# Performance work log

Hardware: AMD Instinct MI355X
Metric: run time of the kernel (lower is better)

Reference implementation:

```python
import jax, jax.numpy as jnp
import numpy as np

DN = ('NCHW', 'OIHW', 'NCHW')

def _conv(x, w, b=None):
    # x: [P, C, H, W], w: [1, C, k, k] -> [P, 1, H, W] with SAME padding
    y = jax.lax.conv_general_dilated(x, w, (1, 1), 'SAME', dimension_numbers=DN)
    if b is not None:
        y = y + b[None, :, None, None]
    return y

def setup_inputs() -> dict:
    key = jax.random.key(0)
    ks = jax.random.split(key, 6)
    T, P, H, W = 36, 64, 128, 256
    K = 5
    inputs = jax.random.normal(ks[0], (T, P, H, W), dtype=jnp.float32)
    w_reset = 0.1 * jax.random.normal(ks[1], (1, 2, K, K), dtype=jnp.float32)
    b_reset = jnp.zeros((1,), dtype=jnp.float32)
    w_update = 0.1 * jax.random.normal(ks[2], (1, 2, K, K), dtype=jnp.float32)
    b_update = jnp.zeros((1,), dtype=jnp.float32)
    w_out = 0.1 * jax.random.normal(ks[3], (1, 2, K, K), dtype=jnp.float32)
    gam = jnp.ones((P,), dtype=jnp.float32)
    add_weights = 0.02 * jax.random.normal(ks[4], (P, H, W), dtype=jnp.float32)
    bias = jnp.zeros((H, W), dtype=jnp.float32)
    return {"inputs": inputs, "w_reset": w_reset, "b_reset": b_reset,
            "w_update": w_update, "b_update": b_update, "w_out": w_out,
            "gam": gam, "add_weights": add_weights, "bias": bias}

def reference(inputs, w_reset, b_reset, w_update, b_update, w_out, gam, add_weights, bias):
    # inputs: [T, P, H, W]; renormalize by per-plant scale gam
    x = gam[None, :, None, None] * inputs
    x = x[:, :, None]  # [T, P, 1, H, W] (channel dim = 1)
    h0 = jnp.zeros_like(x[0])  # [P, 1, H, W]

    def step(h, xt):
        stacked = jnp.concatenate([xt, h], axis=1)  # [P, 2, H, W]
        u = jax.nn.sigmoid(_conv(stacked, w_update, b_update))  # update gate
        r = jax.nn.sigmoid(_conv(stacked, w_reset, b_reset))    # reset gate
        c = _conv(jnp.concatenate([xt, r * h], axis=1), w_out)  # candidate (no bias, no act)
        h_new = h * (1.0 - u) + c * u
        return h_new, h_new

    _, states = jax.lax.scan(step, h0, x)  # [T, P, 1, H, W]
    s = states[:, :, 0]  # [T, P, H, W]
    # final layer (additive=False, rnn_act=None): tanh then per-plant spatial weights
    xs = jnp.tanh(s) * add_weights[None]
    out_y = xs.sum(axis=1) + bias[None]  # [T, H, W]
    return out_y, xs
```

## Files before the change

### kernel.cpp

```cpp
#include <hip/hip_runtime.h>

constexpr int T = 36, P = 64, H = 128, W = 256;
constexpr int HW  = H * W;
constexpr int PHW = P * HW;

constexpr int TH   = 16;
constexpr int NB   = 8;
constexpr int NBLK = P * NB;
constexpr int SR = 25, SC = 268;
constexpr int RR = 20;

constexpr long long TMO_ARRIVE = 3000000;
constexpr long long TMO_STEP   = 1000000;

typedef float vfloat4 __attribute__((ext_vector_type(4)));

__device__ __forceinline__ float fast_sigmoid(float z) {
    float e = __expf(-z);
    return __builtin_amdgcn_rcpf(1.0f + e);
}
__device__ __forceinline__ float fast_tanh(float x) {
    float e = __expf(-2.0f * fabsf(x));
    float t = (1.0f - e) * __builtin_amdgcn_rcpf(1.0f + e);
    return copysignf(t, x);
}

__device__ __forceinline__ void lds_store4(float* d, float4 v) {
    *(float2*)d       = make_float2(v.x, v.y);
    *(float2*)(d + 2) = make_float2(v.z, v.w);
}

__global__ __launch_bounds__(512, 4) void gru_all(
    const float* __restrict__ inputs, const float* __restrict__ gam,
    const float* __restrict__ w_update, const float* __restrict__ b_update,
    const float* __restrict__ w_reset,  const float* __restrict__ b_reset,
    const float* __restrict__ w_out,    const float* __restrict__ add_w,
    float* __restrict__ xs, float* __restrict__ hhalo, int* __restrict__ flags)
{
    __shared__ __align__(16) float sx[SR][SC];
    __shared__ __align__(16) float sh[SR][SC];
    __shared__ __align__(16) float srh[RR][SC];
    __shared__ int s_nowait;

    const int tid  = threadIdx.x;
    const int bid  = blockIdx.x;
    const int p    = bid >> 3;
    const int band = bid & 7;
    const int y0   = band * TH;

    const float gamma = gam[p];
    const float bu = b_update[0];
    const float br = b_reset[0];

    const int cg = tid & 63, rbb = tid >> 6;
    const int ox = 4 * cg,   oy  = 2 * rbb;

    if (tid == 0) {
        s_nowait = 0;
        __hip_atomic_fetch_add(&flags[NBLK], 1, __ATOMIC_RELAXED, __HIP_MEMORY_SCOPE_AGENT);
        const long long t0 = (long long)__builtin_amdgcn_s_memrealtime();
        while (__hip_atomic_load(&flags[NBLK], __ATOMIC_RELAXED, __HIP_MEMORY_SCOPE_AGENT) < NBLK) {
            __builtin_amdgcn_s_sleep(16);
            if ((long long)__builtin_amdgcn_s_memrealtime() - t0 > TMO_ARRIVE) { s_nowait = 1; break; }
        }
    }

    float4 aw4[2];
    #pragma unroll
    for (int k = 0; k < 2; ++k)
        aw4[k] = *(const float4*)&add_w[(size_t)p * HW + (y0 + oy + k) * W + ox];

    for (int s = tid; s < SR * SC; s += 512) {
        (&sx[0][0])[s] = 0.f;
        (&sh[0][0])[s] = 0.f;
    }
    __syncthreads();
    {
        const float* xt = inputs + (size_t)p * HW;
        #pragma unroll
        for (int k = 0; k < 3; ++k) {
            const int s = tid + 512 * k;
            const int r = s >> 6, c4 = s & 63;
            const int gy = y0 + r - 4;
            if ((unsigned)gy < (unsigned)H) {
                float4 v = *(const float4*)&xt[gy * W + 4 * c4];
                v.x *= gamma; v.y *= gamma; v.z *= gamma; v.w *= gamma;
                lds_store4(&sx[r][6 + 4 * c4], v);
            }
        }
    }
    __syncthreads();

    #pragma unroll 1
    for (int t = 0; t < T; ++t) {
        float4 xp[3];
        {
            const int tc = (t + 1 < T) ? t + 1 : t;
            const float* xtn = inputs + (size_t)tc * PHW + (size_t)p * HW;
            #pragma unroll
            for (int k = 0; k < 3; ++k) {
                const int s = tid + 512 * k;
                const int r = s >> 6, c4 = s & 63;
                const int gy = y0 + r - 4;
                xp[k] = make_float4(0.f, 0.f, 0.f, 0.f);
                if ((unsigned)gy < (unsigned)H)
                    xp[k] = *(const float4*)&xtn[gy * W + 4 * c4];
            }
        }

        if (tid < 462) {
            const int b  = tid / 66;
            const int g  = tid - 66 * b;
            const int r0 = 3 * b;
            const int c0 = 4 * g;
            float racc[3][4], hold[3][4];
            #pragma unroll
            for (int k = 0; k < 3; ++k)
                #pragma unroll
                for (int c = 0; c < 4; ++c) racc[k][c] = br;
            #pragma unroll
            for (int ir = 0; ir < 7; ++ir) {
                const float4 xa = *(const float4*)&sx[r0 + ir][c0];
                const float4 xb = *(const float4*)&sx[r0 + ir][c0 + 4];
                const float4 ha = *(const float4*)&sh[r0 + ir][c0];
                const float4 hb = *(const float4*)&sh[r0 + ir][c0 + 4];
                const float vx[8] = {xa.x, xa.y, xa.z, xa.w, xb.x, xb.y, xb.z, xb.w};
                const float vh[8] = {ha.x, ha.y, ha.z, ha.w, hb.x, hb.y, hb.z, hb.w};
                if (ir >= 2 && ir <= 4) {
                    #pragma unroll
                    for (int c = 0; c < 4; ++c) hold[ir - 2][c] = vh[c + 2];
                }
                #pragma unroll
                for (int k = 0; k < 3; ++k) {
                    const int dy = ir - k;
                    if (dy >= 0 && dy <= 4) {
                        #pragma unroll
                        for (int dx = 0; dx < 5; ++dx) {
                            const float wx = w_reset[dy * 5 + dx];
                            const float wh = w_reset[25 + dy * 5 + dx];
                            #pragma unroll
                            for (int c = 0; c < 4; ++c) {
                                racc[k][c] = fmaf(vx[c + dx], wx, racc[k][c]);
                                racc[k][c] = fmaf(vh[c + dx], wh, racc[k][c]);
                            }
                        }
                    }
                }
            }
            #pragma unroll
            for (int k = 0; k < 3; ++k) {
                if (r0 + k < RR) {
                    float4 v;
                    v.x = fast_sigmoid(racc[k][0]) * hold[k][0];
                    v.y = fast_sigmoid(racc[k][1]) * hold[k][1];
                    v.z = fast_sigmoid(racc[k][2]) * hold[k][2];
                    v.w = fast_sigmoid(racc[k][3]) * hold[k][3];
                    lds_store4(&srh[r0 + k][c0 + 2], v);
                }
            }
        }
        __syncthreads();

        float4 hn4[2];
        {
            float uacc[2][4], cacc[2][4], hold[2][4];
            #pragma unroll
            for (int k = 0; k < 2; ++k)
                #pragma unroll
                for (int c = 0; c < 4; ++c) { uacc[k][c] = bu; cacc[k][c] = 0.f; }
            #pragma unroll
            for (int ir = 0; ir < 6; ++ir) {
                const int sr = oy + 2 + ir;
                const float4 xa = *(const float4*)&sx[sr][ox + 4];
                const float4 xb = *(const float4*)&sx[sr][ox + 8];
                const float4 ha = *(const float4*)&sh[sr][ox + 4];
                const float4 hb = *(const float4*)&sh[sr][ox + 8];
                const float4 ra = *(const float4*)&srh[oy + ir][ox + 4];
                const float4 rb = *(const float4*)&srh[oy + ir][ox + 8];
                const float vx[8] = {xa.x, xa.y, xa.z, xa.w, xb.x, xb.y, xb.z, xb.w};
                const float vh[8] = {ha.x, ha.y, ha.z, ha.w, hb.x, hb.y, hb.z, hb.w};
                const float vr[8] = {ra.x, ra.y, ra.z, ra.w, rb.x, rb.y, rb.z, rb.w};
                if (ir == 2) {
                    #pragma unroll
                    for (int c = 0; c < 4; ++c) hold[0][c] = vh[c + 2];
                }
                if (ir == 3) {
                    #pragma unroll
                    for (int c = 0; c < 4; ++c) hold[1][c] = vh[c + 2];
                }
                #pragma unroll
                for (int k = 0; k < 2; ++k) {
                    const int dy = ir - k;
                    if (dy >= 0 && dy <= 4) {
                        #pragma unroll
                        for (int dx = 0; dx < 5; ++dx) {
                            const float wux = w_update[dy * 5 + dx];
                            const float wuh = w_update[25 + dy * 5 + dx];
                            const float wox = w_out[dy * 5 + dx];
                            const float wor = w_out[25 + dy * 5 + dx];
                            #pragma unroll
                            for (int c = 0; c < 4; ++c) {
                                uacc[k][c] = fmaf(vx[c + dx], wux, uacc[k][c]);
                                uacc[k][c] = fmaf(vh[c + dx], wuh, uacc[k][c]);
                                cacc[k][c] = fmaf(vx[c + dx], wox, cacc[k][c]);
                                cacc[k][c] = fmaf(vr[c + dx], wor, cacc[k][c]);
                            }
                        }
                    }
                }
            }
            #pragma unroll
            for (int k = 0; k < 2; ++k) {
                float hn[4];
                #pragma unroll
                for (int c = 0; c < 4; ++c) {
                    const float u = fast_sigmoid(uacc[k][c]);
                    hn[c] = hold[k][c] + (cacc[k][c] - hold[k][c]) * u;
                }
                hn4[k] = make_float4(hn[0], hn[1], hn[2], hn[3]);
            }
        }
        __syncthreads();

        if (t + 1 < T && (rbb < 2 || rbb >= 6)) {
            float* hb = hhalo + (size_t)(t & 1) * (NBLK * 2048) + (size_t)bid * 2048;
            #pragma unroll
            for (int k = 0; k < 2; ++k) {
                const int r    = oy + k;
                const int slot = (r < 4) ? r : r - 8;
                float* d = &hb[slot * 256 + ox];
                __hip_atomic_store(&d[0], hn4[k].x, __ATOMIC_RELAXED, __HIP_MEMORY_SCOPE_AGENT);
                __hip_atomic_store(&d[1], hn4[k].y, __ATOMIC_RELAXED, __HIP_MEMORY_SCOPE_AGENT);
                __hip_atomic_store(&d[2], hn4[k].z, __ATOMIC_RELAXED, __HIP_MEMORY_SCOPE_AGENT);
                __hip_atomic_store(&d[3], hn4[k].w, __ATOMIC_RELAXED, __HIP_MEMORY_SCOPE_AGENT);
            }
        }
        #pragma unroll
        for (int k = 0; k < 2; ++k)
            lds_store4(&sh[4 + oy + k][6 + ox], hn4[k]);
        if (t + 1 < T) {
            #pragma unroll
            for (int k = 0; k < 3; ++k) {
                const int s = tid + 512 * k;
                const int r = s >> 6, c4 = s & 63;
                const int gy = y0 + r - 4;
                if ((unsigned)gy < (unsigned)H) {
                    float4 v = xp[k];
                    v.x *= gamma; v.y *= gamma; v.z *= gamma; v.w *= gamma;
                    lds_store4(&sx[r][6 + 4 * c4], v);
                }
            }
        }
        __syncthreads();

        if (t + 1 < T && tid == 0)
            __hip_atomic_store(&flags[bid], t + 1, __ATOMIC_RELAXED, __HIP_MEMORY_SCOPE_AGENT);
        {
            float* xso = xs + (size_t)t * PHW + (size_t)p * HW;
            #pragma unroll
            for (int k = 0; k < 2; ++k) {
                vfloat4 v;
                v.x = fast_tanh(hn4[k].x) * aw4[k].x;
                v.y = fast_tanh(hn4[k].y) * aw4[k].y;
                v.z = fast_tanh(hn4[k].z) * aw4[k].z;
                v.w = fast_tanh(hn4[k].w) * aw4[k].w;
                __builtin_nontemporal_store(v, (vfloat4*)&xso[(y0 + oy + k) * W + ox]);
            }
        }
        if (t + 1 >= T) break;

        if (tid == 0 || tid == 64) {
            const int dir = (tid == 0) ? -1 : 1;
            const int nbd = band + dir;
            if (nbd >= 0 && nbd < NB && !s_nowait) {
                const int nbid = bid + dir;
                const long long t0 = (long long)__builtin_amdgcn_s_memrealtime();
                while (__hip_atomic_load(&flags[nbid], __ATOMIC_RELAXED, __HIP_MEMORY_SCOPE_AGENT) < t + 1) {
                    __builtin_amdgcn_s_sleep(1);
                    if ((long long)__builtin_amdgcn_s_memrealtime() - t0 > TMO_STEP) { s_nowait = 1; break; }
                }
            }
        }
        __syncthreads();

        {
            float* hb0 = hhalo + (size_t)(t & 1) * (NBLK * 2048);
            const int r = tid >> 6, c4 = tid & 63;
            if (r < 4) {
                if (band > 0) {
                    float* src = &hb0[(size_t)(bid - 1) * 2048 + (4 + r) * 256 + 4 * c4];
                    float4 v;
                    v.x = __hip_atomic_load(&src[0], __ATOMIC_RELAXED, __HIP_MEMORY_SCOPE_AGENT);
                    v.y = __hip_atomic_load(&src[1], __ATOMIC_RELAXED, __HIP_MEMORY_SCOPE_AGENT);
                    v.z = __hip_atomic_load(&src[2], __ATOMIC_RELAXED, __HIP_MEMORY_SCOPE_AGENT);
                    v.w = __hip_atomic_load(&src[3], __ATOMIC_RELAXED, __HIP_MEMORY_SCOPE_AGENT);
                    lds_store4(&sh[r][6 + 4 * c4], v);
                }
            } else {
                if (band < 7) {
                    float* src = &hb0[(size_t)(bid + 1) * 2048 + (r - 4) * 256 + 4 * c4];
                    float4 v;
                    v.x = __hip_atomic_load(&src[0], __ATOMIC_RELAXED, __HIP_MEMORY_SCOPE_AGENT);
                    v.y = __hip_atomic_load(&src[1], __ATOMIC_RELAXED, __HIP_MEMORY_SCOPE_AGENT);
                    v.z = __hip_atomic_load(&src[2], __ATOMIC_RELAXED, __HIP_MEMORY_SCOPE_AGENT);
                    v.w = __hip_atomic_load(&src[3], __ATOMIC_RELAXED, __HIP_MEMORY_SCOPE_AGENT);
                    lds_store4(&sh[16 + r][6 + 4 * c4], v);
                }
            }
        }
        __syncthreads();
    }
}

__global__ __launch_bounds__(256) void reduce_out(
    const float* __restrict__ xs, const float* __restrict__ bias,
    float* __restrict__ out_y)
{
    const int i4  = blockIdx.x * 256 + threadIdx.x;
    const int t   = i4 / (HW / 4);
    const int yx4 = i4 - t * (HW / 4);
    const float4* __restrict__ src = (const float4*)(xs + (size_t)t * PHW) + yx4;
    const float4  b4 = ((const float4*)bias)[yx4];
    float a0[4] = {b4.x, b4.y, b4.z, b4.w};
    float a1[4] = {0.f, 0.f, 0.f, 0.f};
    #pragma unroll 8
    for (int p = 0; p < P; p += 2) {
        const float4 v0 = src[(size_t)p * (HW / 4)];
        const float4 v1 = src[(size_t)(p + 1) * (HW / 4)];
        a0[0] += v0.x; a0[1] += v0.y; a0[2] += v0.z; a0[3] += v0.w;
        a1[0] += v1.x; a1[1] += v1.y; a1[2] += v1.z; a1[3] += v1.w;
    }
    ((float4*)out_y)[i4] = make_float4(a0[0] + a1[0], a0[1] + a1[1],
                                       a0[2] + a1[2], a0[3] + a1[3]);
}

extern "C" void kernel_launch(void* const* d_in, const int* in_sizes, int n_in,
                              void* d_out, int out_size, void* d_ws, size_t ws_size,
                              hipStream_t stream) {
    const float* inputs   = (const float*)d_in[0];
    const float* w_reset  = (const float*)d_in[1];
    const float* b_reset  = (const float*)d_in[2];
    const float* w_update = (const float*)d_in[3];
    const float* b_update = (const float*)d_in[4];
    const float* w_out    = (const float*)d_in[5];
    const float* gam      = (const float*)d_in[6];
    const float* add_w    = (const float*)d_in[7];
    const float* bias     = (const float*)d_in[8];

    float* out_y = (float*)d_out;
    float* xs    = out_y + (size_t)T * HW;

    float* hhalo = (float*)d_ws;
    int*   flags = (int*)((char*)d_ws + (size_t)2 * NBLK * 2048 * sizeof(float));

    (void)hipMemsetAsync(flags, 0, (NBLK + 1) * sizeof(int), stream);

    gru_all<<<dim3(NBLK), dim3(512), 0, stream>>>(
        inputs, gam, w_update, b_update, w_reset, b_reset, w_out, add_w,
        xs, hhalo, flags);

    const int nout4 = T * HW / 4;
    reduce_out<<<nout4 / 256, 256, 0, stream>>>(xs, bias, out_y);
}
```

Before: 897.2 us.

## Replace block-level step flags with per-wave halo counters and drop register prefetch

Each band now has separate top and bottom halo flags. The two waves that write halo rows wait for their own stores (vmcnt(0)) and then atomically increment a counter, which removes the __syncthreads that preceded the single per-block flag store. Neighbours poll for a count of 2*(t+1). Halo stores are also skipped for edge bands that have no neighbour. The next-timestep input prefetch into registers is removed, so inputs are loaded directly when sx is refilled. This frees registers but puts the global load latency on the critical path.

```diff
diff --git a/kernel.cpp b/kernel.cpp
--- a/kernel.cpp
+++ b/kernel.cpp
@@ -55,11 +55,14 @@
     const int cg = tid & 63, rbb = tid >> 6;
     const int ox = 4 * cg,   oy  = 2 * rbb;
 
+    int* flagsTop = flags;
+    int* flagsBot = flags + NBLK;
+
     if (tid == 0) {
         s_nowait = 0;
-        __hip_atomic_fetch_add(&flags[NBLK], 1, __ATOMIC_RELAXED, __HIP_MEMORY_SCOPE_AGENT);
+        __hip_atomic_fetch_add(&flags[2 * NBLK], 1, __ATOMIC_RELAXED, __HIP_MEMORY_SCOPE_AGENT);
         const long long t0 = (long long)__builtin_amdgcn_s_memrealtime();
-        while (__hip_atomic_load(&flags[NBLK], __ATOMIC_RELAXED, __HIP_MEMORY_SCOPE_AGENT) < NBLK) {
+        while (__hip_atomic_load(&flags[2 * NBLK], __ATOMIC_RELAXED, __HIP_MEMORY_SCOPE_AGENT) < NBLK) {
             __builtin_amdgcn_s_sleep(16);
             if ((long long)__builtin_amdgcn_s_memrealtime() - t0 > TMO_ARRIVE) { s_nowait = 1; break; }
         }
@@ -93,21 +96,6 @@
 
     #pragma unroll 1
     for (int t = 0; t < T; ++t) {
-        float4 xp[3];
-        {
-            const int tc = (t + 1 < T) ? t + 1 : t;
-            const float* xtn = inputs + (size_t)tc * PHW + (size_t)p * HW;
-            #pragma unroll
-            for (int k = 0; k < 3; ++k) {
-                const int s = tid + 512 * k;
-                const int r = s >> 6, c4 = s & 63;
-                const int gy = y0 + r - 4;
-                xp[k] = make_float4(0.f, 0.f, 0.f, 0.f);
-                if ((unsigned)gy < (unsigned)H)
-                    xp[k] = *(const float4*)&xtn[gy * W + 4 * c4];
-            }
-        }
-
         if (tid < 462) {
             const int b  = tid / 66;
             const int g  = tid - 66 * b;
@@ -222,39 +210,54 @@
         }
         __syncthreads();
 
-        if (t + 1 < T && (rbb < 2 || rbb >= 6)) {
-            float* hb = hhalo + (size_t)(t & 1) * (NBLK * 2048) + (size_t)bid * 2048;
-            #pragma unroll
-            for (int k = 0; k < 2; ++k) {
-                const int r    = oy + k;
-                const int slot = (r < 4) ? r : r - 8;
-                float* d = &hb[slot * 256 + ox];
-                __hip_atomic_store(&d[0], hn4[k].x, __ATOMIC_RELAXED, __HIP_MEMORY_SCOPE_AGENT);
-                __hip_atomic_store(&d[1], hn4[k].y, __ATOMIC_RELAXED, __HIP_MEMORY_SCOPE_AGENT);
-                __hip_atomic_store(&d[2], hn4[k].z, __ATOMIC_RELAXED, __HIP_MEMORY_SCOPE_AGENT);
-                __hip_atomic_store(&d[3], hn4[k].w, __ATOMIC_RELAXED, __HIP_MEMORY_SCOPE_AGENT);
-            }
-        }
+        if (t + 1 < T) {
+            if (rbb < 2 && band > 0) {
+                float* hb = hhalo + (size_t)(t & 1) * (NBLK * 2048) + (size_t)bid * 2048;
+                #pragma unroll
+                for (int k = 0; k < 2; ++k) {
+                    float* d = &hb[(oy + k) * 256 + ox];
+                    __hip_atomic_store(&d[0], hn4[k].x, __ATOMIC_RELAXED, __HIP_MEMORY_SCOPE_AGENT);
+                    __hip_atomic_store(&d[1], hn4[k].y, __ATOMIC_RELAXED, __HIP_MEMORY_SCOPE_AGENT);
+                    __hip_atomic_store(&d[2], hn4[k].z, __ATOMIC_RELAXED, __HIP_MEMORY_SCOPE_AGENT);
+                    __hip_atomic_store(&d[3], hn4[k].w, __ATOMIC_RELAXED, __HIP_MEMORY_SCOPE_AGENT);
+                }
+                asm volatile("s_waitcnt vmcnt(0)" ::: "memory");
+                if (cg == 0)
+                    __hip_atomic_fetch_add(&flagsTop[bid], 1, __ATOMIC_RELAXED, __HIP_MEMORY_SCOPE_AGENT);
+            }
+            if (rbb >= 6 && band < 7) {
+                float* hb = hhalo + (size_t)(t & 1) * (NBLK * 2048) + (size_t)bid * 2048;
+                #pragma unroll
+                for (int k = 0; k < 2; ++k) {
+                    float* d = &hb[(oy + k - 8) * 256 + ox];
+                    __hip_atomic_store(&d[0], hn4[k].x, __ATOMIC_RELAXED, __HIP_MEMORY_SCOPE_AGENT);
+                    __hip_atomic_store(&d[1], hn4[k].y, __ATOMIC_RELAXED, __HIP_MEMORY_SCOPE_AGENT);
+                    __hip_atomic_store(&d[2], hn4[k].z, __ATOMIC_RELAXED, __HIP_MEMORY_SCOPE_AGENT);
+                    __hip_atomic_store(&d[3], hn4[k].w, __ATOMIC_RELAXED, __HIP_MEMORY_SCOPE_AGENT);
+                }
+                asm volatile("s_waitcnt vmcnt(0)" ::: "memory");
+                if (cg == 0)
+                    __hip_atomic_fetch_add(&flagsBot[bid], 1, __ATOMIC_RELAXED, __HIP_MEMORY_SCOPE_AGENT);
+            }
+        }
+
         #pragma unroll
         for (int k = 0; k < 2; ++k)
             lds_store4(&sh[4 + oy + k][6 + ox], hn4[k]);
         if (t + 1 < T) {
+            const float* xt = inputs + (size_t)(t + 1) * PHW + (size_t)p * HW;
             #pragma unroll
             for (int k = 0; k < 3; ++k) {
                 const int s = tid + 512 * k;
                 const int r = s >> 6, c4 = s & 63;
                 const int gy = y0 + r - 4;
                 if ((unsigned)gy < (unsigned)H) {
-                    float4 v = xp[k];
+                    float4 v = *(const float4*)&xt[gy * W + 4 * c4];
                     v.x *= gamma; v.y *= gamma; v.z *= gamma; v.w *= gamma;
                     lds_store4(&sx[r][6 + 4 * c4], v);
                 }
             }
         }
-        __syncthreads();
-
-        if (t + 1 < T && tid == 0)
-            __hip_atomic_store(&flags[bid], t + 1, __ATOMIC_RELAXED, __HIP_MEMORY_SCOPE_AGENT);
         {
             float* xso = xs + (size_t)t * PHW + (size_t)p * HW;
             #pragma unroll
@@ -269,16 +272,18 @@
         }
         if (t + 1 >= T) break;
 
-        if (tid == 0 || tid == 64) {
-            const int dir = (tid == 0) ? -1 : 1;
-            const int nbd = band + dir;
-            if (nbd >= 0 && nbd < NB && !s_nowait) {
-                const int nbid = bid + dir;
-                const long long t0 = (long long)__builtin_amdgcn_s_memrealtime();
-                while (__hip_atomic_load(&flags[nbid], __ATOMIC_RELAXED, __HIP_MEMORY_SCOPE_AGENT) < t + 1) {
-                    __builtin_amdgcn_s_sleep(1);
-                    if ((long long)__builtin_amdgcn_s_memrealtime() - t0 > TMO_STEP) { s_nowait = 1; break; }
-                }
+        if (tid == 0 && band > 0 && !s_nowait) {
+            const long long t0 = (long long)__builtin_amdgcn_s_memrealtime();
+            while (__hip_atomic_load(&flagsBot[bid - 1], __ATOMIC_RELAXED, __HIP_MEMORY_SCOPE_AGENT) < 2 * (t + 1)) {
+                __builtin_amdgcn_s_sleep(1);
+                if ((long long)__builtin_amdgcn_s_memrealtime() - t0 > TMO_STEP) { s_nowait = 1; break; }
+            }
+        }
+        if (tid == 64 && band < 7 && !s_nowait) {
+            const long long t0 = (long long)__builtin_amdgcn_s_memrealtime();
+            while (__hip_atomic_load(&flagsTop[bid + 1], __ATOMIC_RELAXED, __HIP_MEMORY_SCOPE_AGENT) < 2 * (t + 1)) {
+                __builtin_amdgcn_s_sleep(1);
+                if ((long long)__builtin_amdgcn_s_memrealtime() - t0 > TMO_STEP) { s_nowait = 1; break; }
             }
         }
         __syncthreads();
@@ -353,7 +358,7 @@
     float* hhalo = (float*)d_ws;
     int*   flags = (int*)((char*)d_ws + (size_t)2 * NBLK * 2048 * sizeof(float));
 
-    (void)hipMemsetAsync(flags, 0, (NBLK + 1) * sizeof(int), stream);
+    (void)hipMemsetAsync(flags, 0, (2 * NBLK + 1) * sizeof(int), stream);
 
     gru_all<<<dim3(NBLK), dim3(512), 0, stream>>>(
         inputs, gam, w_update, b_update, w_reset, b_reset, w_out, add_w,
```

Measured after the change: 773.9 us. -13.7%, faster.
